# Kernel tuning notes

Hardware: AMD Instinct MI355X
Metric: run time of the kernel (lower is better)

The kernel has to match this reference:

```python
import jax, jax.numpy as jnp
import numpy as np

E, B, T = 7, 50, 100               # ensemble (network_size), no_batches=50, time blocks
D, A, L, H, C = 128, 32, 256, 1024, 128  # data, action, latent, hidden, context sizes
H_STEP = 0.1                        # (t1 - t0) / T == dt -> one SDE step per block


def setup_inputs() -> dict:
    key = jax.random.key(0)
    ks = iter(jax.random.split(key, 64))
    def nrm(shape, scale=1.0):
        return jax.random.normal(next(ks), shape, jnp.float32) * scale
    def ens(i, o):
        s = 1.0 / np.sqrt(i)
        return nrm((E, i, o), s), nrm((E, o), s)
    def lin(i, o):
        s = 1.0 / np.sqrt(i)
        return nrm((i, o), s), nrm((o,), s)
    inp = {}
    inp["enc_w1"], inp["enc_b1"] = ens(D, H)
    inp["enc_w2"], inp["enc_b2"] = ens(H, H)
    inp["enc_w3"], inp["enc_b3"] = ens(H, C)
    inp["qz0_w"], inp["qz0_b"] = ens(C, 2 * L)
    inp["act_w"], inp["act_b"] = ens(L + A + D, L)
    inp["proj_w1"], inp["proj_b1"] = ens(L, H)
    inp["proj_w2"], inp["proj_b2"] = ens(H, H)
    inp["proj_w3"], inp["proj_b3"] = ens(H, D)
    inp["f_w1"], inp["f_b1"] = lin(L, H)
    inp["f_w2"], inp["f_b2"] = lin(H, H)
    inp["f_w3"], inp["f_b3"] = lin(H, L)
    inp["h_w1"], inp["h_b1"] = lin(L, H)
    inp["h_w2"], inp["h_b2"] = lin(H, H)
    inp["h_w3"], inp["h_b3"] = lin(H, L)
    # per-latent-dim g nets: Linear(1,H) -> ReLU -> Linear(H,1), stacked over L dims
    inp["g_w1"] = nrm((L, H), 0.2)
    inp["g_b1"] = nrm((L, H), 0.2)
    inp["g_w2"] = nrm((L, H), 0.2 / np.sqrt(H))
    inp["g_b2"] = 0.5 + nrm((L,), 0.01)   # keep diffusion bounded away from 0
    inp["pz0_mean"] = jnp.zeros((E, 1, L), jnp.float32)
    inp["pz0_logstd"] = jnp.zeros((E, 1, L), jnp.float32)
    inp["xs"] = nrm((E, T * B, D))
    inp["actions"] = nrm((E, T * B, A))
    inp["eps_z0"] = nrm((T, E, B, L))      # torch.randn_like noise for z0 reparam
    inp["dw_noise"] = nrm((T, E * B, L))   # Brownian increment noise (unit std)
    return inp


def reference(enc_w1, enc_b1, enc_w2, enc_b2, enc_w3, enc_b3,
              qz0_w, qz0_b, act_w, act_b,
              proj_w1, proj_b1, proj_w2, proj_b2, proj_w3, proj_b3,
              f_w1, f_b1, f_w2, f_b2, f_w3, f_b3,
              h_w1, h_b1, h_w2, h_b2, h_w3, h_b3,
              g_w1, g_b1, g_w2, g_b2,
              pz0_mean, pz0_logstd,
              xs, actions, eps_z0, dw_noise):
    def ens_lin(x, w, b):  # EnsembleFC: bmm + bias
        return jnp.einsum('ebi,eio->ebo', x, w) + b[:, None, :]

    def encoder(x):
        x = jax.nn.relu(ens_lin(x, enc_w1, enc_b1))
        x = jax.nn.relu(ens_lin(x, enc_w2, enc_b2))
        return ens_lin(x, enc_w3, enc_b3)

    def projector(z):
        z = jnp.tanh(ens_lin(z, proj_w1, proj_b1))
        z = jnp.tanh(ens_lin(z, proj_w2, proj_b2))
        return ens_lin(z, proj_w3, proj_b3)

    def mlp(y, w1, b1, w2, b2, w3, b3):  # Linear-ReLU-Linear-Tanh-Linear
        y = jax.nn.relu(y @ w1 + b1)
        y = jnp.tanh(y @ w2 + b2)
        return y @ w3 + b3

    def g_fn(y):  # vectorized per-dim tiny MLPs: y (N, L) -> (N, L)
        hh = jax.nn.relu(y[:, :, None] * g_w1[None] + g_b1[None])  # (N, L, H)
        return jnp.sum(hh * g_w2[None], axis=-1) + g_b2

    xs_t = jnp.moveaxis(xs.reshape(E, T, B, D), 1, 0)        # (T, E, B, D)
    act_t = jnp.moveaxis(actions.reshape(E, T, B, A), 1, 0)  # (T, E, B, A)
    sqrt_h = jnp.sqrt(jnp.float32(H_STEP))

    def step(carry, inps):
        zs_last, i = carry
        x_i, a_i, eps_i, dw_i = inps
        ctx = encoder(x_i)                                  # (E, B, C)
        q = ens_lin(ctx, qz0_w, qz0_b)                      # (E, B, 2L)
        qm, ql = q[..., :L], q[..., L:]
        z0 = qm + jnp.exp(ql) * eps_i
        z_in = jnp.where(i == 0, z0, zs_last)               # first step uses z0
        lad = jnp.concatenate([z_in, a_i, x_i], axis=2)
        z = ens_lin(lad, act_w, act_b).reshape(E * B, L)
        # one SDE step with logqp (f: posterior drift, h: prior drift, g: diffusion)
        fv = mlp(z, f_w1, f_b1, f_w2, f_b2, f_w3, f_b3)
        hv = mlp(z, h_w1, h_b1, h_w2, h_b2, h_w3, h_b3)
        gv = g_fn(z)
        u = (fv - hv) / gv
        lr = 0.5 * jnp.sum(u * u, axis=-1) * H_STEP         # (E*B,) log-ratio increment
        z_new = z + fv * H_STEP + gv * (sqrt_h * dw_i)
        zs_new = z_new.reshape(E, B, L)
        xm = projector(zs_new)                              # (E, B, D)
        # KL(q(z0) || p(z0)) for diagonal Gaussians
        kl = (pz0_logstd - ql) \
             + (jnp.exp(2.0 * ql) + (qm - pz0_mean) ** 2) / (2.0 * jnp.exp(2.0 * pz0_logstd)) \
             - 0.5
        logqp0 = kl.sum(axis=2).mean(axis=1)                # (E,)
        lr_mean = lr.reshape(E, B).mean(axis=1)             # (E,)
        return (zs_new, i + 1), (lr_mean, logqp0, xm)

    init = (jnp.zeros((E, B, L), xs.dtype), jnp.int32(0))
    (_, _), (lrm, lq0, xms) = jax.lax.scan(step, init, (xs_t, act_t, eps_z0, dw_noise))
    logqp_path = lrm.sum(axis=0) + lq0.sum(axis=0)          # (E,)
    predicted_xs = jnp.moveaxis(xms, 0, 1).reshape(E, T * B, D)
    return logqp_path, predicted_xs
```

## Files before the change

### kernel.cpp

```cpp
#include <hip/hip_runtime.h>
#include <hip/hip_bf16.h>
#include <math.h>

#define E_ 7
#define B_ 50
#define T_ 100
#define D_ 128
#define A_ 32
#define L_ 256
#define H_ 1024
#define C_ 128
#define LAD_ 416
#define EB_ 350
#define TB_ 5000
#define SQRTH 0.31622776601683794f

typedef __attribute__((ext_vector_type(8))) short s8v;
typedef __attribute__((ext_vector_type(4))) float f32x4;
typedef __hip_bfloat16 bf16;

struct BG {
  const bf16* A[8];
  const bf16* W[8];
  const float* bias[8];
  float* Cf[8];
  bf16* Cb[8];
};

template<int BM, int ACT, int OUT>
__global__ __launch_bounds__(256)
void bgemm(BG g, int M, int K, int lda, int ldw, int ldc) {
  __shared__ short As[BM * 64];
  __shared__ short Ws[128 * 64];
  const short* Ap = (const short*)g.A[blockIdx.z];
  const short* Wp = (const short*)g.W[blockIdx.z];
  const int bm = blockIdx.x * BM, bn = blockIdx.y * 128;
  const int tid = threadIdx.x;
  const int wv = tid >> 6, lane = tid & 63;
  const int wm0 = (wv >> 1) * (BM / 2), wn0 = (wv & 1) * 64;
  const int l15 = lane & 15, l4 = lane >> 4;
  constexpr int FM = BM / 32;
  constexpr int AI = BM / 32;
  f32x4 acc[FM][4] = {};
  for (int k0 = 0; k0 < K; k0 += 64) {
    s8v av[AI], wvv[4];
#pragma unroll
    for (int i = 0; i < AI; ++i) {
      const int c = tid + i * 256, r = c >> 3, ck = c & 7;
      s8v v = {};
      if (bm + r < M) v = *(const s8v*)(Ap + (size_t)(bm + r) * lda + k0 + ck * 8);
      av[i] = v;
    }
#pragma unroll
    for (int i = 0; i < 4; ++i) {
      const int c = tid + i * 256, r = c >> 3, ck = c & 7;
      wvv[i] = *(const s8v*)(Wp + (size_t)(bn + r) * ldw + k0 + ck * 8);
    }
    __syncthreads();
#pragma unroll
    for (int i = 0; i < AI; ++i) {
      const int c = tid + i * 256, r = c >> 3, ck = c & 7;
      *(s8v*)(As + r * 64 + ((ck ^ (r & 7)) << 3)) = av[i];
    }
#pragma unroll
    for (int i = 0; i < 4; ++i) {
      const int c = tid + i * 256, r = c >> 3, ck = c & 7;
      *(s8v*)(Ws + r * 64 + ((ck ^ (r & 7)) << 3)) = wvv[i];
    }
    __syncthreads();
#pragma unroll
    for (int ks = 0; ks < 2; ++ks) {
      s8v af[FM], bfr[4];
#pragma unroll
      for (int m = 0; m < FM; ++m) {
        const int r = wm0 + m * 16 + l15, ck = ks * 4 + l4;
        af[m] = *(const s8v*)(As + r * 64 + ((ck ^ (r & 7)) << 3));
      }
#pragma unroll
      for (int n = 0; n < 4; ++n) {
        const int r = wn0 + n * 16 + l15, ck = ks * 4 + l4;
        bfr[n] = *(const s8v*)(Ws + r * 64 + ((ck ^ (r & 7)) << 3));
      }
#pragma unroll
      for (int m = 0; m < FM; ++m)
#pragma unroll
        for (int n = 0; n < 4; ++n)
          acc[m][n] = __builtin_amdgcn_mfma_f32_16x16x32_bf16(af[m], bfr[n], acc[m][n], 0, 0, 0);
    }
    __syncthreads();
  }
  const float* bias = g.bias[blockIdx.z];
  float* Cf = g.Cf[blockIdx.z];
  bf16* Cb = g.Cb[blockIdx.z];
#pragma unroll
  for (int n = 0; n < 4; ++n) {
    const int col = bn + wn0 + n * 16 + l15;
    const float bv = bias ? bias[col] : 0.f;
#pragma unroll
    for (int m = 0; m < FM; ++m) {
#pragma unroll
      for (int j = 0; j < 4; ++j) {
        const int row = bm + wm0 + m * 16 + l4 * 4 + j;
        if (row < M) {
          float v = acc[m][n][j] + bv;
          if (ACT == 1) v = fmaxf(v, 0.f);
          if (ACT == 2) v = tanhf(v);
          if (OUT == 0) Cf[(size_t)row * ldc + col] = v;
          if (OUT == 1) Cb[(size_t)row * ldc + col] = __float2bfloat16(v);
        }
      }
    }
  }
}

__global__ __launch_bounds__(256)
void cvtT_kernel(const float* __restrict__ src, bf16* __restrict__ dst,
                 int K, int N, long ss, long ds) {
  __shared__ float t[32][33];
  src += (size_t)blockIdx.z * ss;
  dst += (size_t)blockIdx.z * ds;
  const int n0 = blockIdx.x * 32, k0 = blockIdx.y * 32;
  const int tx = threadIdx.x & 31, ty = threadIdx.x >> 5;
#pragma unroll
  for (int i = 0; i < 4; ++i)
    t[ty + 8 * i][tx] = src[(size_t)(k0 + ty + 8 * i) * N + n0 + tx];
  __syncthreads();
#pragma unroll
  for (int i = 0; i < 4; ++i)
    dst[(size_t)(n0 + ty + 8 * i) * K + k0 + tx] = __float2bfloat16(t[tx][ty + 8 * i]);
}

struct B4 { bf16 a, b, c, d; };
__global__ __launch_bounds__(256)
void cvt_kernel(const float* __restrict__ s, bf16* __restrict__ d, int n4) {
  const int i = blockIdx.x * 256 + threadIdx.x;
  if (i < n4) {
    const float4 v = ((const float4*)s)[i];
    B4 o = {__float2bfloat16(v.x), __float2bfloat16(v.y),
            __float2bfloat16(v.z), __float2bfloat16(v.w)};
    ((B4*)d)[i] = o;
  }
}

__global__ __launch_bounds__(256)
void act_gemm(const float* __restrict__ zin, int zin_estride,
              const float* __restrict__ actions, const float* __restrict__ xs,
              const float* __restrict__ act_w, const float* __restrict__ act_b,
              float* __restrict__ zout, bf16* __restrict__ zout_bf, int t) {
  __shared__ float As[16][68];
  __shared__ float Bs[16][64];
  const int tid = threadIdx.x;
  const int e = blockIdx.y;
  const int bn = blockIdx.x * 64;
  const int tm = (tid >> 4) << 2;
  const int tn = (tid & 15) << 2;
  const int am = tid >> 2;
  const int ak = (tid & 3) << 2;
  const int bk = tid >> 4;
  const int bn4 = (tid & 15) << 2;
  const float* W = act_w + (size_t)e * LAD_ * L_;
  const float* zin_e = zin + (size_t)e * zin_estride;
  float acc[4][4] = {};
  for (int k0 = 0; k0 < LAD_; k0 += 16) {
    float4 av = make_float4(0.f, 0.f, 0.f, 0.f);
    const int k = k0 + ak;
    if (am < B_) {
      if (k < L_)
        av = *(const float4*)(zin_e + (size_t)am * L_ + k);
      else if (k < L_ + A_)
        av = *(const float4*)(actions + ((size_t)e * TB_ + (size_t)t * B_ + am) * A_ + (k - L_));
      else
        av = *(const float4*)(xs + ((size_t)e * TB_ + (size_t)t * B_ + am) * D_ + (k - L_ - A_));
    }
    const float4 wv = *(const float4*)(W + (size_t)(k0 + bk) * L_ + (bn + bn4));
    __syncthreads();
    As[ak + 0][am] = av.x; As[ak + 1][am] = av.y;
    As[ak + 2][am] = av.z; As[ak + 3][am] = av.w;
    *(float4*)&Bs[bk][bn4] = wv;
    __syncthreads();
#pragma unroll
    for (int kk = 0; kk < 16; ++kk) {
      const float4 a4 = *(const float4*)&As[kk][tm];
      const float4 b4 = *(const float4*)&Bs[kk][tn];
      const float ar[4] = {a4.x, a4.y, a4.z, a4.w};
      const float br[4] = {b4.x, b4.y, b4.z, b4.w};
#pragma unroll
      for (int i = 0; i < 4; ++i)
#pragma unroll
        for (int j = 0; j < 4; ++j)
          acc[i][j] = fmaf(ar[i], br[j], acc[i][j]);
    }
  }
#pragma unroll
  for (int i = 0; i < 4; ++i) {
    const int m = tm + i;
    if (m < B_) {
#pragma unroll
      for (int j = 0; j < 4; ++j) {
        const float v = acc[i][j] + act_b[(size_t)e * L_ + bn + tn + j];
        const size_t idx = ((size_t)e * B_ + m) * L_ + (bn + tn + j);
        zout[idx] = v;
        zout_bf[idx] = __float2bfloat16(v);
      }
    }
  }
}

__global__ __launch_bounds__(256)
void qkl_kernel(const float* __restrict__ ctx, int rows, int row_off, int ctx_estride,
                const float* __restrict__ qw, const float* __restrict__ qb,
                const float* __restrict__ pm, const float* __restrict__ pl,
                const float* __restrict__ eps0, float* __restrict__ z0,
                float* __restrict__ logqp) {
  __shared__ float cx[16][128];
  __shared__ float red[16];
  const int e = blockIdx.y;
  const int r0 = blockIdx.x * 16;
  const int tid = threadIdx.x;
  {
    const int r = tid >> 4, c = (tid & 15) * 8;
    float4 v0 = make_float4(0.f, 0.f, 0.f, 0.f), v1 = v0;
    if (r0 + r < rows) {
      const float* src = ctx + (size_t)e * ctx_estride + (size_t)(r0 + r) * C_ + c;
      v0 = *(const float4*)src;
      v1 = *(const float4*)(src + 4);
    }
    *(float4*)&cx[r][c] = v0;
    *(float4*)&cx[r][c + 4] = v1;
  }
  if (tid < 16) red[tid] = 0.f;
  __syncthreads();
  const int j = tid;
  const float* w = qw + (size_t)e * C_ * 512;
  float am_[16] = {};
  float al_[16] = {};
  for (int k0 = 0; k0 < C_; k0 += 4) {
    float wm[4], wl[4];
#pragma unroll
    for (int q = 0; q < 4; ++q) {
      wm[q] = w[(size_t)(k0 + q) * 512 + j];
      wl[q] = w[(size_t)(k0 + q) * 512 + 256 + j];
    }
#pragma unroll
    for (int r = 0; r < 16; ++r) {
      const float4 cv = *(const float4*)&cx[r][k0];
      const float cc[4] = {cv.x, cv.y, cv.z, cv.w};
#pragma unroll
      for (int q = 0; q < 4; ++q) {
        am_[r] = fmaf(cc[q], wm[q], am_[r]);
        al_[r] = fmaf(cc[q], wl[q], al_[r]);
      }
    }
  }
  const float qbm = qb[(size_t)e * 512 + j];
  const float qbl = qb[(size_t)e * 512 + 256 + j];
  const float pmv = pm[(size_t)e * L_ + j];
  const float plv = pl[(size_t)e * L_ + j];
  const float inv2e = 0.5f * expf(-2.f * plv);
#pragma unroll
  for (int r = 0; r < 16; ++r) {
    float kl = 0.f;
    if (r0 + r < rows) {
      const float qm_ = am_[r] + qbm;
      const float ql_ = al_[r] + qbl;
      const float dm = qm_ - pmv;
      kl = plv - ql_ + (expf(2.f * ql_) + dm * dm) * inv2e - 0.5f;
      const int gi = row_off + r0 + r;
      if (gi < B_) {
        const size_t zi = ((size_t)e * B_ + gi) * L_ + j;
        z0[zi] = qm_ + expf(ql_) * eps0[zi];
      }
    }
    for (int off = 32; off; off >>= 1) kl += __shfl_xor(kl, off, 64);
    if ((tid & 63) == 0) atomicAdd(&red[r], kl);
  }
  __syncthreads();
  if (tid < 16 && r0 + tid < rows) atomicAdd(&logqp[e], red[tid] * (1.0f / B_));
}

__global__ __launch_bounds__(64)
void g_kernel(const float* __restrict__ z, const float* __restrict__ gw1,
              const float* __restrict__ gb1, const float* __restrict__ gw2,
              const float* __restrict__ gb2, float* __restrict__ gv) {
  const int l = blockIdx.x;
  const int r0 = blockIdx.y * 44;
  const int rend = (r0 + 44 < EB_) ? (r0 + 44) : EB_;
  const int lane = threadIdx.x;
  float w1[16], b1[16], w2[16];
#pragma unroll
  for (int i = 0; i < 16; ++i) {
    const int h = lane + i * 64;
    w1[i] = gw1[(size_t)l * H_ + h];
    b1[i] = gb1[(size_t)l * H_ + h];
    w2[i] = gw2[(size_t)l * H_ + h];
  }
  const float g2 = gb2[l];
  for (int r = r0; r < rend; ++r) {
    const float zv = z[(size_t)r * L_ + l];
    float acc = 0.f;
#pragma unroll
    for (int i = 0; i < 16; ++i) {
      float hh = fmaf(zv, w1[i], b1[i]);
      hh = fmaxf(hh, 0.f);
      acc = fmaf(hh, w2[i], acc);
    }
    for (int off = 32; off; off >>= 1) acc += __shfl_xor(acc, off, 64);
    if (lane == 0) gv[(size_t)r * L_ + l] = acc + g2;
  }
}

__global__ __launch_bounds__(256)
void epi_kernel(const float* __restrict__ fvp, const float* __restrict__ fb3,
                const float* __restrict__ hb3, const float* __restrict__ gv,
                const float* __restrict__ z, const float* __restrict__ dw,
                float* __restrict__ zs_all, bf16* __restrict__ zs_bf,
                float* __restrict__ logqp, int t) {
  __shared__ float wsum[4];
  const int r = blockIdx.x;
  const int l = threadIdx.x;
  const int e = r / B_, b = r - e * B_;
  const size_t rl = (size_t)r * L_ + l;
  float fv = fb3[l], hv = hb3[l];
#pragma unroll
  for (int s = 0; s < 4; ++s) {
    fv += fvp[(size_t)s * EB_ * L_ + rl];
    hv += fvp[(size_t)(4 + s) * EB_ * L_ + rl];
  }
  const float gvv = gv[rl];
  const float u = (fv - hv) / gvv;
  float s_ = u * u;
  for (int off = 32; off; off >>= 1) s_ += __shfl_xor(s_, off, 64);
  if ((l & 63) == 0) wsum[l >> 6] = s_;
  __syncthreads();
  if (l == 0) {
    const float tot = wsum[0] + wsum[1] + wsum[2] + wsum[3];
    atomicAdd(&logqp[e], 0.5f * tot * 0.1f * (1.0f / B_));
  }
  const float znew = z[rl] + fv * 0.1f + gvv * (SQRTH * dw[(size_t)t * EB_ * L_ + rl]);
  const size_t oi = (((size_t)e * T_ + t) * B_ + b) * L_ + l;
  zs_all[oi] = znew;
  zs_bf[oi] = __float2bfloat16(znew);
}

__global__ void init_kernel(float* logqp) {
  if (threadIdx.x < E_) logqp[threadIdx.x] = 0.f;
}

extern "C" void kernel_launch(void* const* d_in, const int* in_sizes, int n_in,
                              void* d_out, int out_size, void* d_ws, size_t ws_size,
                              hipStream_t stream) {
  (void)in_sizes; (void)n_in; (void)out_size;
  const float* enc_w1 = (const float*)d_in[0];
  const float* enc_b1 = (const float*)d_in[1];
  const float* enc_w2 = (const float*)d_in[2];
  const float* enc_b2 = (const float*)d_in[3];
  const float* enc_w3 = (const float*)d_in[4];
  const float* enc_b3 = (const float*)d_in[5];
  const float* qz0_w  = (const float*)d_in[6];
  const float* qz0_b  = (const float*)d_in[7];
  const float* act_w  = (const float*)d_in[8];
  const float* act_b  = (const float*)d_in[9];
  const float* proj_w1 = (const float*)d_in[10];
  const float* proj_b1 = (const float*)d_in[11];
  const float* proj_w2 = (const float*)d_in[12];
  const float* proj_b2 = (const float*)d_in[13];
  const float* proj_w3 = (const float*)d_in[14];
  const float* proj_b3 = (const float*)d_in[15];
  const float* f_w1 = (const float*)d_in[16];
  const float* f_b1 = (const float*)d_in[17];
  const float* f_w2 = (const float*)d_in[18];
  const float* f_b2 = (const float*)d_in[19];
  const float* f_w3 = (const float*)d_in[20];
  const float* f_b3 = (const float*)d_in[21];
  const float* h_w1 = (const float*)d_in[22];
  const float* h_b1 = (const float*)d_in[23];
  const float* h_w2 = (const float*)d_in[24];
  const float* h_b2 = (const float*)d_in[25];
  const float* h_w3 = (const float*)d_in[26];
  const float* h_b3 = (const float*)d_in[27];
  const float* g_w1 = (const float*)d_in[28];
  const float* g_b1 = (const float*)d_in[29];
  const float* g_w2 = (const float*)d_in[30];
  const float* g_b2 = (const float*)d_in[31];
  const float* pz0_mean   = (const float*)d_in[32];
  const float* pz0_logstd = (const float*)d_in[33];
  const float* xs      = (const float*)d_in[34];
  const float* actions = (const float*)d_in[35];
  const float* eps_z0  = (const float*)d_in[36];
  const float* dw      = (const float*)d_in[37];

  float* out = (float*)d_out;
  float* logqp = out;
  float* pred = out + E_;

  char* base = (char*)d_ws;
  size_t off = 0;
  auto alloc = [&](size_t bytes) {
    void* p = base + off;
    off = (off + bytes + 255) & ~(size_t)255;
    return p;
  };
  float* zs_all = (float*)alloc((size_t)E_ * T_ * B_ * L_ * 4);
  bf16* zs_bf   = (bf16*)alloc((size_t)E_ * T_ * B_ * L_ * 2);
  float* z0     = (float*)alloc((size_t)E_ * B_ * L_ * 4);
  float* zbuf   = (float*)alloc((size_t)EB_ * L_ * 4);
  bf16* zbuf_bf = (bf16*)alloc((size_t)EB_ * L_ * 2);
  bf16* fh1     = (bf16*)alloc((size_t)2 * EB_ * H_ * 2);
  bf16* fh2     = (bf16*)alloc((size_t)2 * EB_ * H_ * 2);
  float* fvhvp  = (float*)alloc((size_t)8 * EB_ * L_ * 4);
  float* gvb    = (float*)alloc((size_t)EB_ * L_ * 4);
  bf16* xs_bf   = (bf16*)alloc((size_t)E_ * TB_ * D_ * 2);
  bf16* ew1T = (bf16*)alloc((size_t)E_ * D_ * H_ * 2);
  bf16* ew2T = (bf16*)alloc((size_t)E_ * H_ * H_ * 2);
  bf16* ew3T = (bf16*)alloc((size_t)E_ * H_ * C_ * 2);
  bf16* pw1T = (bf16*)alloc((size_t)E_ * L_ * H_ * 2);
  bf16* pw2T = (bf16*)alloc((size_t)E_ * H_ * H_ * 2);
  bf16* pw3T = (bf16*)alloc((size_t)E_ * H_ * D_ * 2);
  bf16* fw1T = (bf16*)alloc((size_t)L_ * H_ * 2);
  bf16* fw2T = (bf16*)alloc((size_t)H_ * H_ * 2);
  bf16* fw3T = (bf16*)alloc((size_t)H_ * L_ * 2);
  bf16* hw1T = (bf16*)alloc((size_t)L_ * H_ * 2);
  bf16* hw2T = (bf16*)alloc((size_t)H_ * H_ * 2);
  bf16* hw3T = (bf16*)alloc((size_t)H_ * L_ * 2);
  const size_t per_row = (size_t)E_ * (H_ * 2 * 2 + C_ * 4);
  size_t remain = (ws_size > off + 4096) ? (ws_size - off - 4096) : 0;
  int CH = (int)(remain / per_row);
  if (CH > 2500) CH = 2500;
  if (CH < 64) CH = 64;
  bf16* bufA = (bf16*)alloc((size_t)E_ * CH * H_ * 2);
  bf16* bufB = (bf16*)alloc((size_t)E_ * CH * H_ * 2);
  float* bufC = (float*)alloc((size_t)E_ * CH * C_ * 4);

  init_kernel<<<dim3(1), dim3(64), 0, stream>>>(logqp);

  const dim3 cb(256);
  cvt_kernel<<<dim3((E_ * TB_ * D_ / 4 + 255) / 256), cb, 0, stream>>>(xs, xs_bf, E_ * TB_ * D_ / 4);
  cvtT_kernel<<<dim3(H_ / 32, D_ / 32, E_), cb, 0, stream>>>(enc_w1, ew1T, D_, H_, (long)D_ * H_, (long)D_ * H_);
  cvtT_kernel<<<dim3(H_ / 32, H_ / 32, E_), cb, 0, stream>>>(enc_w2, ew2T, H_, H_, (long)H_ * H_, (long)H_ * H_);
  cvtT_kernel<<<dim3(C_ / 32, H_ / 32, E_), cb, 0, stream>>>(enc_w3, ew3T, H_, C_, (long)H_ * C_, (long)H_ * C_);
  cvtT_kernel<<<dim3(H_ / 32, L_ / 32, E_), cb, 0, stream>>>(proj_w1, pw1T, L_, H_, (long)L_ * H_, (long)L_ * H_);
  cvtT_kernel<<<dim3(H_ / 32, H_ / 32, E_), cb, 0, stream>>>(proj_w2, pw2T, H_, H_, (long)H_ * H_, (long)H_ * H_);
  cvtT_kernel<<<dim3(D_ / 32, H_ / 32, E_), cb, 0, stream>>>(proj_w3, pw3T, H_, D_, (long)H_ * D_, (long)H_ * D_);
  cvtT_kernel<<<dim3(H_ / 32, L_ / 32, 1), cb, 0, stream>>>(f_w1, fw1T, L_, H_, 0, 0);
  cvtT_kernel<<<dim3(H_ / 32, H_ / 32, 1), cb, 0, stream>>>(f_w2, fw2T, H_, H_, 0, 0);
  cvtT_kernel<<<dim3(L_ / 32, H_ / 32, 1), cb, 0, stream>>>(f_w3, fw3T, H_, L_, 0, 0);
  cvtT_kernel<<<dim3(H_ / 32, L_ / 32, 1), cb, 0, stream>>>(h_w1, hw1T, L_, H_, 0, 0);
  cvtT_kernel<<<dim3(H_ / 32, H_ / 32, 1), cb, 0, stream>>>(h_w2, hw2T, H_, H_, 0, 0);
  cvtT_kernel<<<dim3(L_ / 32, H_ / 32, 1), cb, 0, stream>>>(h_w3, hw3T, H_, L_, 0, 0);

  BG g;
  for (int c = 0; c < TB_; c += CH) {
    const int rows = (TB_ - c < CH) ? (TB_ - c) : CH;
    const int mt = (rows + 127) / 128;
    for (int e = 0; e < E_; ++e) {
      g.A[e] = xs_bf + ((size_t)e * TB_ + c) * D_;
      g.W[e] = ew1T + (size_t)e * D_ * H_;
      g.bias[e] = enc_b1 + (size_t)e * H_;
      g.Cb[e] = bufA + (size_t)e * CH * H_;
    }
    bgemm<128, 1, 1><<<dim3(mt, H_ / 128, E_), 256, 0, stream>>>(g, rows, D_, D_, D_, H_);
    for (int e = 0; e < E_; ++e) {
      g.A[e] = bufA + (size_t)e * CH * H_;
      g.W[e] = ew2T + (size_t)e * H_ * H_;
      g.bias[e] = enc_b2 + (size_t)e * H_;
      g.Cb[e] = bufB + (size_t)e * CH * H_;
    }
    bgemm<128, 1, 1><<<dim3(mt, H_ / 128, E_), 256, 0, stream>>>(g, rows, H_, H_, H_, H_);
    for (int e = 0; e < E_; ++e) {
      g.A[e] = bufB + (size_t)e * CH * H_;
      g.W[e] = ew3T + (size_t)e * H_ * C_;
      g.bias[e] = enc_b3 + (size_t)e * C_;
      g.Cf[e] = bufC + (size_t)e * CH * C_;
    }
    bgemm<128, 0, 0><<<dim3(mt, C_ / 128, E_), 256, 0, stream>>>(g, rows, H_, H_, H_, C_);
    qkl_kernel<<<dim3((rows + 15) / 16, E_), 256, 0, stream>>>(
        bufC, rows, c, CH * C_, qz0_w, qz0_b, pz0_mean, pz0_logstd, eps_z0, z0, logqp);
  }

  for (int t = 0; t < T_; ++t) {
    const float* zin;
    int zes;
    if (t == 0) { zin = z0; zes = B_ * L_; }
    else { zin = zs_all + (size_t)(t - 1) * B_ * L_; zes = T_ * B_ * L_; }
    act_gemm<<<dim3(L_ / 64, E_), 256, 0, stream>>>(zin, zes, actions, xs, act_w, act_b,
                                                    zbuf, zbuf_bf, t);
    g.A[0] = zbuf_bf; g.W[0] = fw1T; g.bias[0] = f_b1; g.Cb[0] = fh1;
    g.A[1] = zbuf_bf; g.W[1] = hw1T; g.bias[1] = h_b1; g.Cb[1] = fh1 + (size_t)EB_ * H_;
    bgemm<64, 1, 1><<<dim3(6, H_ / 128, 2), 256, 0, stream>>>(g, EB_, L_, L_, L_, H_);
    g.A[0] = fh1; g.W[0] = fw2T; g.bias[0] = f_b2; g.Cb[0] = fh2;
    g.A[1] = fh1 + (size_t)EB_ * H_; g.W[1] = hw2T; g.bias[1] = h_b2;
    g.Cb[1] = fh2 + (size_t)EB_ * H_;
    bgemm<64, 2, 1><<<dim3(6, H_ / 128, 2), 256, 0, stream>>>(g, EB_, H_, H_, H_, H_);
    for (int jj = 0; jj < 8; ++jj) {
      const int fb = jj >> 2, s = jj & 3;
      g.A[jj] = fh2 + (size_t)fb * EB_ * H_ + s * 256;
      g.W[jj] = (fb ? hw3T : fw3T) + s * 256;
      g.bias[jj] = nullptr;
      g.Cf[jj] = fvhvp + (size_t)jj * EB_ * L_;
    }
    bgemm<64, 0, 0><<<dim3(6, L_ / 128, 8), 256, 0, stream>>>(g, EB_, 256, H_, H_, L_);
    g_kernel<<<dim3(L_, 8), 64, 0, stream>>>(zbuf, g_w1, g_b1, g_w2, g_b2, gvb);
    epi_kernel<<<dim3(EB_), 256, 0, stream>>>(fvhvp, f_b3, h_b3, gvb, zbuf, dw,
                                              zs_all, zs_bf, logqp, t);
  }

  for (int c = 0; c < TB_; c += CH) {
    const int rows = (TB_ - c < CH) ? (TB_ - c) : CH;
    const int mt = (rows + 127) / 128;
    for (int e = 0; e < E_; ++e) {
      g.A[e] = zs_bf + ((size_t)e * T_ * B_ + c) * L_;
      g.W[e] = pw1T + (size_t)e * L_ * H_;
      g.bias[e] = proj_b1 + (size_t)e * H_;
      g.Cb[e] = bufA + (size_t)e * CH * H_;
    }
    bgemm<128, 2, 1><<<dim3(mt, H_ / 128, E_), 256, 0, stream>>>(g, rows, L_, L_, L_, H_);
    for (int e = 0; e < E_; ++e) {
      g.A[e] = bufA + (size_t)e * CH * H_;
      g.W[e] = pw2T + (size_t)e * H_ * H_;
      g.bias[e] = proj_b2 + (size_t)e * H_;
      g.Cb[e] = bufB + (size_t)e * CH * H_;
    }
    bgemm<128, 2, 1><<<dim3(mt, H_ / 128, E_), 256, 0, stream>>>(g, rows, H_, H_, H_, H_);
    for (int e = 0; e < E_; ++e) {
      g.A[e] = bufB + (size_t)e * CH * H_;
      g.W[e] = pw3T + (size_t)e * H_ * D_;
      g.bias[e] = proj_b3 + (size_t)e * D_;
      g.Cf[e] = pred + ((size_t)e * TB_ + c) * D_;
    }
    bgemm<128, 0, 0><<<dim3(mt, D_ / 128, E_), 256, 0, stream>>>(g, rows, H_, H_, H_, D_);
  }
}
```

Measured before the change: 11.16 ms.

## Restructure SDE time loop into four fused MFMA kernels with prepacked weights

Rewrites the per-timestep loop. The action/xs part of the action projection is precomputed for all timesteps with one batched GEMM. The z part uses split-bf16 (hi/lo) MFMA to keep near-fp32 accuracy. The f and h MLP layers are concatenated into single wide GEMMs over fragment-prepacked weights, and layer 3, the per-dim g network (fp16 packed), the log-ratio and the Euler update are fused into one kernel. This cuts per-step launches from six to four and removes the intermediate fvhvp/gv buffers, at the cost of more precomputation and lower-precision g evaluation.

```diff
diff --git a/kernel.cpp b/kernel.cpp
--- a/kernel.cpp
+++ b/kernel.cpp
@@ -10,14 +10,20 @@
 #define L_ 256
 #define H_ 1024
 #define C_ 128
-#define LAD_ 416
 #define EB_ 350
 #define TB_ 5000
 #define SQRTH 0.31622776601683794f
 
 typedef __attribute__((ext_vector_type(8))) short s8v;
 typedef __attribute__((ext_vector_type(4))) float f32x4;
+typedef _Float16 f16x2 __attribute__((ext_vector_type(2)));
 typedef __hip_bfloat16 bf16;
+
+#define MFMA __builtin_amdgcn_mfma_f32_16x16x32_bf16
+
+__device__ __forceinline__ int lswz(int row, int ck) {
+  return ((ck & ~7) | ((ck ^ row) & 7)) << 3;
+}
 
 struct BG {
   const bf16* A[8];
@@ -85,7 +91,7 @@
       for (int m = 0; m < FM; ++m)
 #pragma unroll
         for (int n = 0; n < 4; ++n)
-          acc[m][n] = __builtin_amdgcn_mfma_f32_16x16x32_bf16(af[m], bfr[n], acc[m][n], 0, 0, 0);
+          acc[m][n] = MFMA(af[m], bfr[n], acc[m][n], 0, 0, 0);
     }
     __syncthreads();
   }
@@ -143,75 +149,69 @@
 }
 
 __global__ __launch_bounds__(256)
-void act_gemm(const float* __restrict__ zin, int zin_estride,
-              const float* __restrict__ actions, const float* __restrict__ xs,
-              const float* __restrict__ act_w, const float* __restrict__ act_b,
-              float* __restrict__ zout, bf16* __restrict__ zout_bf, int t) {
-  __shared__ float As[16][68];
-  __shared__ float Bs[16][64];
-  const int tid = threadIdx.x;
-  const int e = blockIdx.y;
-  const int bn = blockIdx.x * 64;
-  const int tm = (tid >> 4) << 2;
-  const int tn = (tid & 15) << 2;
-  const int am = tid >> 2;
-  const int ak = (tid & 3) << 2;
-  const int bk = tid >> 4;
-  const int bn4 = (tid & 15) << 2;
-  const float* W = act_w + (size_t)e * LAD_ * L_;
-  const float* zin_e = zin + (size_t)e * zin_estride;
-  float acc[4][4] = {};
-  for (int k0 = 0; k0 < LAD_; k0 += 16) {
-    float4 av = make_float4(0.f, 0.f, 0.f, 0.f);
-    const int k = k0 + ak;
-    if (am < B_) {
-      if (k < L_)
-        av = *(const float4*)(zin_e + (size_t)am * L_ + k);
-      else if (k < L_ + A_)
-        av = *(const float4*)(actions + ((size_t)e * TB_ + (size_t)t * B_ + am) * A_ + (k - L_));
-      else
-        av = *(const float4*)(xs + ((size_t)e * TB_ + (size_t)t * B_ + am) * D_ + (k - L_ - A_));
-    }
-    const float4 wv = *(const float4*)(W + (size_t)(k0 + bk) * L_ + (bn + bn4));
-    __syncthreads();
-    As[ak + 0][am] = av.x; As[ak + 1][am] = av.y;
-    As[ak + 2][am] = av.z; As[ak + 3][am] = av.w;
-    *(float4*)&Bs[bk][bn4] = wv;
-    __syncthreads();
-#pragma unroll
-    for (int kk = 0; kk < 16; ++kk) {
-      const float4 a4 = *(const float4*)&As[kk][tm];
-      const float4 b4 = *(const float4*)&Bs[kk][tn];
-      const float ar[4] = {a4.x, a4.y, a4.z, a4.w};
-      const float br[4] = {b4.x, b4.y, b4.z, b4.w};
-#pragma unroll
-      for (int i = 0; i < 4; ++i)
-#pragma unroll
-        for (int j = 0; j < 4; ++j)
-          acc[i][j] = fmaf(ar[i], br[j], acc[i][j]);
-    }
-  }
-#pragma unroll
-  for (int i = 0; i < 4; ++i) {
-    const int m = tm + i;
-    if (m < B_) {
-#pragma unroll
-      for (int j = 0; j < 4; ++j) {
-        const float v = acc[i][j] + act_b[(size_t)e * L_ + bn + tn + j];
-        const size_t idx = ((size_t)e * B_ + m) * L_ + (bn + tn + j);
-        zout[idx] = v;
-        zout_bf[idx] = __float2bfloat16(v);
-      }
-    }
-  }
+void packW(const float* __restrict__ src, bf16* __restrict__ dst, int K, int N) {
+  const int idx = blockIdx.x * 256 + threadIdx.x;
+  if (idx >= K * N) return;
+  const int k = idx / N, n = idx - k * N;
+  const size_t fo = ((size_t)(n >> 4) * (K >> 5) + (k >> 5)) * 512 +
+                    (((k >> 3) & 3) << 7) + ((n & 15) << 3) + (k & 7);
+  dst[fo] = __float2bfloat16(src[idx]);
+}
+
+__global__ __launch_bounds__(256)
+void packWz(const float* __restrict__ act_w, bf16* __restrict__ hi, bf16* __restrict__ lo) {
+  const int idx = blockIdx.x * 256 + threadIdx.x;
+  if (idx >= E_ * 65536) return;
+  const int e = idx >> 16, rem = idx & 65535, k = rem >> 8, n = rem & 255;
+  const float w = act_w[(size_t)e * 416 * 256 + (size_t)k * 256 + n];
+  const bf16 h = __float2bfloat16(w);
+  const size_t fo = (size_t)e * 65536 + ((size_t)(n >> 4) * 8 + (k >> 5)) * 512 +
+                    (((k >> 3) & 3) << 7) + ((n & 15) << 3) + (k & 7);
+  hi[fo] = h;
+  lo[fo] = __float2bfloat16(w - __bfloat162float(h));
+}
+
+__global__ __launch_bounds__(256)
+void ax_build(const float* __restrict__ actions, const float* __restrict__ xs,
+              bf16* __restrict__ dst) {
+  const int idx = blockIdx.x * 256 + threadIdx.x;
+  if (idx >= E_ * TB_ * 192) return;
+  const int k = idx % 192;
+  const int r = (idx / 192) % TB_;
+  const int e = idx / (192 * TB_);
+  float v = 0.f;
+  if (k < 32) v = actions[((size_t)e * TB_ + r) * A_ + k];
+  else if (k < 160) v = xs[((size_t)e * TB_ + r) * D_ + (k - 32)];
+  dst[idx] = __float2bfloat16(v);
+}
+
+__global__ __launch_bounds__(256)
+void waxT_build(const float* __restrict__ act_w, bf16* __restrict__ dst) {
+  const int idx = blockIdx.x * 256 + threadIdx.x;
+  if (idx >= E_ * 256 * 192) return;
+  const int k = idx % 192;
+  const int n = (idx / 192) % 256;
+  const int e = idx / (192 * 256);
+  float v = (k < 160) ? act_w[(size_t)e * 416 * 256 + (size_t)(256 + k) * 256 + n] : 0.f;
+  dst[idx] = __float2bfloat16(v);
+}
+
+__global__ __launch_bounds__(256)
+void gpack_build(const float* __restrict__ gw1, const float* __restrict__ gb1,
+                 const float* __restrict__ gw2, _Float16* __restrict__ dst) {
+  const int idx = blockIdx.x * 256 + threadIdx.x;
+  if (idx >= 256 * 3 * 1024) return;
+  const int l = idx / 3072, rem = idx - l * 3072, arr = rem >> 10, h = rem & 1023;
+  const float* s = arr == 0 ? gw1 : (arr == 1 ? gb1 : gw2);
+  dst[idx] = (_Float16)s[(size_t)l * 1024 + h];
 }
 
 __global__ __launch_bounds__(256)
 void qkl_kernel(const float* __restrict__ ctx, int rows, int row_off, int ctx_estride,
                 const float* __restrict__ qw, const float* __restrict__ qb,
                 const float* __restrict__ pm, const float* __restrict__ pl,
-                const float* __restrict__ eps0, float* __restrict__ z0,
-                float* __restrict__ logqp) {
+                const float* __restrict__ eps0, bf16* __restrict__ z0hi,
+                bf16* __restrict__ z0lo, float* __restrict__ logqp) {
   __shared__ float cx[16][128];
   __shared__ float red[16];
   const int e = blockIdx.y;
@@ -268,7 +268,10 @@
       const int gi = row_off + r0 + r;
       if (gi < B_) {
         const size_t zi = ((size_t)e * B_ + gi) * L_ + j;
-        z0[zi] = qm_ + expf(ql_) * eps0[zi];
+        const float z0 = qm_ + expf(ql_) * eps0[zi];
+        const bf16 h = __float2bfloat16(z0);
+        z0hi[zi] = h;
+        z0lo[zi] = __float2bfloat16(z0 - __bfloat162float(h));
       }
     }
     for (int off = 32; off; off >>= 1) kl += __shfl_xor(kl, off, 64);
@@ -278,68 +281,266 @@
   if (tid < 16 && r0 + tid < rows) atomicAdd(&logqp[e], red[tid] * (1.0f / B_));
 }
 
-__global__ __launch_bounds__(64)
-void g_kernel(const float* __restrict__ z, const float* __restrict__ gw1,
-              const float* __restrict__ gb1, const float* __restrict__ gw2,
-              const float* __restrict__ gb2, float* __restrict__ gv) {
-  const int l = blockIdx.x;
-  const int r0 = blockIdx.y * 44;
-  const int rend = (r0 + 44 < EB_) ? (r0 + 44) : EB_;
-  const int lane = threadIdx.x;
-  float w1[16], b1[16], w2[16];
-#pragma unroll
-  for (int i = 0; i < 16; ++i) {
-    const int h = lane + i * 64;
-    w1[i] = gw1[(size_t)l * H_ + h];
-    b1[i] = gb1[(size_t)l * H_ + h];
-    w2[i] = gw2[(size_t)l * H_ + h];
-  }
-  const float g2 = gb2[l];
-  for (int r = r0; r < rend; ++r) {
-    const float zv = z[(size_t)r * L_ + l];
-    float acc = 0.f;
-#pragma unroll
-    for (int i = 0; i < 16; ++i) {
-      float hh = fmaf(zv, w1[i], b1[i]);
-      hh = fmaxf(hh, 0.f);
-      acc = fmaf(hh, w2[i], acc);
-    }
-    for (int off = 32; off; off >>= 1) acc += __shfl_xor(acc, off, 64);
-    if (lane == 0) gv[(size_t)r * L_ + l] = acc + g2;
-  }
-}
-
-__global__ __launch_bounds__(256)
-void epi_kernel(const float* __restrict__ fvp, const float* __restrict__ fb3,
-                const float* __restrict__ hb3, const float* __restrict__ gv,
-                const float* __restrict__ z, const float* __restrict__ dw,
-                float* __restrict__ zs_all, bf16* __restrict__ zs_bf,
-                float* __restrict__ logqp, int t) {
-  __shared__ float wsum[4];
-  const int r = blockIdx.x;
-  const int l = threadIdx.x;
-  const int e = r / B_, b = r - e * B_;
-  const size_t rl = (size_t)r * L_ + l;
-  float fv = fb3[l], hv = hb3[l];
-#pragma unroll
-  for (int s = 0; s < 4; ++s) {
-    fv += fvp[(size_t)s * EB_ * L_ + rl];
-    hv += fvp[(size_t)(4 + s) * EB_ * L_ + rl];
-  }
-  const float gvv = gv[rl];
-  const float u = (fv - hv) / gvv;
-  float s_ = u * u;
-  for (int off = 32; off; off >>= 1) s_ += __shfl_xor(s_, off, 64);
-  if ((l & 63) == 0) wsum[l >> 6] = s_;
-  __syncthreads();
-  if (l == 0) {
-    const float tot = wsum[0] + wsum[1] + wsum[2] + wsum[3];
-    atomicAdd(&logqp[e], 0.5f * tot * 0.1f * (1.0f / B_));
-  }
-  const float znew = z[rl] + fv * 0.1f + gvv * (SQRTH * dw[(size_t)t * EB_ * L_ + rl]);
-  const size_t oi = (((size_t)e * T_ + t) * B_ + b) * L_ + l;
-  zs_all[oi] = znew;
-  zs_bf[oi] = __float2bfloat16(znew);
+__global__ __launch_bounds__(256, 2)
+void k1_act(const bf16* __restrict__ zhi, const bf16* __restrict__ zlo,
+            const bf16* __restrict__ wzh, const bf16* __restrict__ wzl,
+            const float* __restrict__ axw, float* __restrict__ zP,
+            bf16* __restrict__ zPb, int t) {
+  __shared__ short Ah[16 * 256];
+  __shared__ short Al[16 * 256];
+  const int e = blockIdx.z, rb = blockIdx.x, nb = blockIdx.y * 128;
+  const int r0 = rb * 13;
+  const int nrows = (50 - r0 < 13) ? (50 - r0) : 13;
+  const int tid = threadIdx.x, lane = tid & 63, wv = tid >> 6;
+  const int l15 = lane & 15, l4 = lane >> 4;
+  const short* zh = (const short*)zhi + (size_t)(e * 50 + r0) * 256;
+  const short* zl = (const short*)zlo + (size_t)(e * 50 + r0) * 256;
+#pragma unroll
+  for (int i = 0; i < 2; ++i) {
+    const int lin = tid + i * 256, row = lin >> 5, ck = lin & 31;
+    s8v vh = {}, vl = {};
+    if (row < nrows) {
+      vh = *(const s8v*)(zh + row * 256 + ck * 8);
+      vl = *(const s8v*)(zl + row * 256 + ck * 8);
+    }
+    *(s8v*)(Ah + row * 256 + lswz(row, ck)) = vh;
+    *(s8v*)(Al + row * 256 + lswz(row, ck)) = vl;
+  }
+  __syncthreads();
+  const short* Bh = (const short*)wzh + (size_t)e * 65536;
+  const short* Bl = (const short*)wzl + (size_t)e * 65536;
+  f32x4 acc[2] = {};
+#pragma unroll
+  for (int kt = 0; kt < 8; ++kt) {
+    const int ck = kt * 4 + l4;
+    const s8v ah = *(const s8v*)(Ah + l15 * 256 + lswz(l15, ck));
+    const s8v al = *(const s8v*)(Al + l15 * 256 + lswz(l15, ck));
+#pragma unroll
+    for (int nt = 0; nt < 2; ++nt) {
+      const int ng = nb + wv * 32 + nt * 16;
+      const size_t bo = ((size_t)(ng >> 4) * 8 + kt) * 512 + lane * 8;
+      const s8v bh = *(const s8v*)(Bh + bo);
+      const s8v bl = *(const s8v*)(Bl + bo);
+      acc[nt] = MFMA(ah, bh, acc[nt], 0, 0, 0);
+      acc[nt] = MFMA(al, bh, acc[nt], 0, 0, 0);
+      acc[nt] = MFMA(ah, bl, acc[nt], 0, 0, 0);
+    }
+  }
+#pragma unroll
+  for (int nt = 0; nt < 2; ++nt) {
+    const int col = nb + wv * 32 + nt * 16 + l15;
+#pragma unroll
+    for (int j = 0; j < 4; ++j) {
+      const int row = l4 * 4 + j;
+      if (row < nrows) {
+        const int gr = e * 50 + r0 + row;
+        const float v = acc[nt][j] + axw[((size_t)e * TB_ + t * 50 + r0 + row) * 256 + col];
+        zP[(size_t)gr * 256 + col] = v;
+        zPb[(size_t)gr * 256 + col] = __float2bfloat16(v);
+      }
+    }
+  }
+}
+
+__global__ __launch_bounds__(256, 2)
+void k2_l1(const bf16* __restrict__ zPb, const bf16* __restrict__ w1f,
+           const float* __restrict__ fb1, const float* __restrict__ hb1,
+           bf16* __restrict__ fh1) {
+  __shared__ short As[16 * 256];
+  const int rb = blockIdx.x, nb = blockIdx.y * 128;
+  const int r0 = rb * 16;
+  const int tid = threadIdx.x, lane = tid & 63, wv = tid >> 6;
+  const int l15 = lane & 15, l4 = lane >> 4;
+#pragma unroll
+  for (int i = 0; i < 2; ++i) {
+    const int lin = tid + i * 256, row = lin >> 5, ck = lin & 31;
+    s8v v = {};
+    if (r0 + row < EB_)
+      v = *(const s8v*)((const short*)zPb + (size_t)(r0 + row) * 256 + ck * 8);
+    *(s8v*)(As + row * 256 + lswz(row, ck)) = v;
+  }
+  __syncthreads();
+  f32x4 acc[2] = {};
+#pragma unroll
+  for (int kt = 0; kt < 8; ++kt) {
+    const int ck = kt * 4 + l4;
+    const s8v a = *(const s8v*)(As + l15 * 256 + lswz(l15, ck));
+#pragma unroll
+    for (int nt = 0; nt < 2; ++nt) {
+      const int ng = nb + wv * 32 + nt * 16;
+      const s8v b = *(const s8v*)((const short*)w1f + ((size_t)(ng >> 4) * 8 + kt) * 512 + lane * 8);
+      acc[nt] = MFMA(a, b, acc[nt], 0, 0, 0);
+    }
+  }
+#pragma unroll
+  for (int nt = 0; nt < 2; ++nt) {
+    const int col = nb + wv * 32 + nt * 16 + l15;
+    const float bv = (col < 1024) ? fb1[col] : hb1[col - 1024];
+#pragma unroll
+    for (int j = 0; j < 4; ++j) {
+      const int row = r0 + l4 * 4 + j;
+      if (row < EB_)
+        fh1[(size_t)row * 2048 + col] = __float2bfloat16(fmaxf(acc[nt][j] + bv, 0.f));
+    }
+  }
+}
+
+__global__ __launch_bounds__(256, 2)
+void k3_l2(const bf16* __restrict__ fh1, const bf16* __restrict__ w2f,
+           const float* __restrict__ fb2, const float* __restrict__ hb2,
+           bf16* __restrict__ fh2) {
+  __shared__ short As[16 * 1024];
+  const int rb = blockIdx.x, nbl = blockIdx.y;
+  const int nb = nbl * 128, r0 = rb * 16;
+  const int half = (nbl >= 8) ? 1024 : 0;
+  const int tid = threadIdx.x, lane = tid & 63, wv = tid >> 6;
+  const int l15 = lane & 15, l4 = lane >> 4;
+#pragma unroll
+  for (int i = 0; i < 8; ++i) {
+    const int lin = tid + i * 256, row = lin >> 7, ck = lin & 127;
+    s8v v = {};
+    if (r0 + row < EB_)
+      v = *(const s8v*)((const short*)fh1 + (size_t)(r0 + row) * 2048 + half + ck * 8);
+    *(s8v*)(As + row * 1024 + lswz(row, ck)) = v;
+  }
+  __syncthreads();
+  f32x4 acc[2] = {};
+#pragma unroll 4
+  for (int kt = 0; kt < 32; ++kt) {
+    const int ck = kt * 4 + l4;
+    const s8v a = *(const s8v*)(As + l15 * 1024 + lswz(l15, ck));
+#pragma unroll
+    for (int nt = 0; nt < 2; ++nt) {
+      const int ng = nb + wv * 32 + nt * 16;
+      const s8v b = *(const s8v*)((const short*)w2f + ((size_t)(ng >> 4) * 32 + kt) * 512 + lane * 8);
+      acc[nt] = MFMA(a, b, acc[nt], 0, 0, 0);
+    }
+  }
+#pragma unroll
+  for (int nt = 0; nt < 2; ++nt) {
+    const int col = nb + wv * 32 + nt * 16 + l15;
+    const float bv = half ? hb2[col - 1024] : fb2[col];
+#pragma unroll
+    for (int j = 0; j < 4; ++j) {
+      const int row = r0 + l4 * 4 + j;
+      if (row < EB_)
+        fh2[(size_t)row * 2048 + col] = __float2bfloat16(tanhf(acc[nt][j] + bv));
+    }
+  }
+}
+
+__global__ __launch_bounds__(256, 1)
+void k4_fin(const bf16* __restrict__ fh2, const bf16* __restrict__ w3f,
+            const float* __restrict__ fb3, const float* __restrict__ hb3,
+            const _Float16* __restrict__ gpk, const float* __restrict__ gb2,
+            const float* __restrict__ zP, const float* __restrict__ dw,
+            bf16* __restrict__ zhi, bf16* __restrict__ zlo,
+            bf16* __restrict__ zs_bf, float* __restrict__ logqp, int t) {
+  __shared__ short As[16 * 1024];
+  __shared__ float ztile[16][64];
+  __shared__ float gvt[16][64];
+  __shared__ float ebuck[8];
+  const int rb = blockIdx.x, cb = blockIdx.y;
+  const int r0 = rb * 16, c0 = cb * 64;
+  const int tid = threadIdx.x, lane = tid & 63, wv = tid >> 6;
+  const int l15 = lane & 15, l4 = lane >> 4;
+  if (tid < 8) ebuck[tid] = 0.f;
+#pragma unroll
+  for (int i = 0; i < 4; ++i) {
+    const int lin = tid + i * 256, row = lin >> 6, col = lin & 63;
+    ztile[row][col] = (r0 + row < EB_) ? zP[(size_t)(r0 + row) * 256 + c0 + col] : 1.0f;
+  }
+  f32x4 accF = {}, accH = {};
+#pragma unroll
+  for (int fb = 0; fb < 2; ++fb) {
+    __syncthreads();
+#pragma unroll
+    for (int i = 0; i < 8; ++i) {
+      const int lin = tid + i * 256, row = lin >> 7, ck = lin & 127;
+      s8v v = {};
+      if (r0 + row < EB_)
+        v = *(const s8v*)((const short*)fh2 + (size_t)(r0 + row) * 2048 + fb * 1024 + ck * 8);
+      *(s8v*)(As + row * 1024 + lswz(row, ck)) = v;
+    }
+    __syncthreads();
+    const int ng = fb * 256 + c0 + wv * 16;
+    f32x4 acc = {};
+#pragma unroll 4
+    for (int kt = 0; kt < 32; ++kt) {
+      const int ck = kt * 4 + l4;
+      const s8v a = *(const s8v*)(As + l15 * 1024 + lswz(l15, ck));
+      const s8v b = *(const s8v*)((const short*)w3f + ((size_t)(ng >> 4) * 32 + kt) * 512 + lane * 8);
+      acc = MFMA(a, b, acc, 0, 0, 0);
+    }
+    if (fb) accH = acc; else accF = acc;
+  }
+  __syncthreads();
+  {
+    const int lloc = tid >> 2, hq = tid & 3;
+    const _Float16* gl = gpk + (size_t)(c0 + lloc) * 3072 + hq * 256;
+    f16x2 z2[16];
+#pragma unroll
+    for (int r = 0; r < 16; ++r) {
+      const _Float16 zh_ = (_Float16)ztile[r][lloc];
+      z2[r] = f16x2{zh_, zh_};
+    }
+    float ga[16] = {};
+    for (int hp = 0; hp < 128; ++hp) {
+      const f16x2 w1v = *(const f16x2*)(gl + 2 * hp);
+      const f16x2 b1v = *(const f16x2*)(gl + 1024 + 2 * hp);
+      const f16x2 w2v = *(const f16x2*)(gl + 2048 + 2 * hp);
+#pragma unroll
+      for (int r = 0; r < 16; ++r) {
+        f16x2 tt = z2[r] * w1v + b1v;
+#if __has_builtin(__builtin_elementwise_max)
+        const f16x2 zz = {};
+        tt = __builtin_elementwise_max(tt, zz);
+#else
+        tt[0] = tt[0] > (_Float16)0 ? tt[0] : (_Float16)0;
+        tt[1] = tt[1] > (_Float16)0 ? tt[1] : (_Float16)0;
+#endif
+#if __has_builtin(__builtin_amdgcn_fdot2)
+        ga[r] = __builtin_amdgcn_fdot2(tt, w2v, ga[r], false);
+#else
+        ga[r] += (float)tt[0] * (float)w2v[0] + (float)tt[1] * (float)w2v[1];
+#endif
+      }
+    }
+#pragma unroll
+    for (int r = 0; r < 16; ++r) {
+      float v = ga[r];
+      v += __shfl_xor(v, 1, 64);
+      v += __shfl_xor(v, 2, 64);
+      if (hq == 0) gvt[r][lloc] = v + gb2[c0 + lloc];
+    }
+  }
+  __syncthreads();
+  const int col_loc = wv * 16 + l15, col = c0 + col_loc;
+  const float fb3v = fb3[col], hb3v = hb3[col];
+#pragma unroll
+  for (int j = 0; j < 4; ++j) {
+    const int rl = l4 * 4 + j, row = r0 + rl;
+    if (row < EB_) {
+      const float fv = accF[j] + fb3v;
+      const float hv = accH[j] + hb3v;
+      const float gv = gvt[rl][col_loc];
+      const float u = (fv - hv) / gv;
+      atomicAdd(&ebuck[row / 50], 0.001f * u * u);
+      const float znew = ztile[rl][col_loc] + 0.1f * fv +
+                         gv * (SQRTH * dw[(size_t)t * (EB_ * 256) + (size_t)row * 256 + col]);
+      const bf16 h = __float2bfloat16(znew);
+      const size_t zi = (size_t)row * 256 + col;
+      zhi[zi] = h;
+      zlo[zi] = __float2bfloat16(znew - __bfloat162float(h));
+      const int e = row / 50, b = row - e * 50;
+      zs_bf[((size_t)e * TB_ + t * 50 + b) * 256 + col] = h;
+    }
+  }
+  __syncthreads();
+  if (tid < 7) {
+    const float v = ebuck[tid];
+    if (v != 0.f) atomicAdd(&logqp[tid], v);
+  }
 }
 
 __global__ void init_kernel(float* logqp) {
@@ -400,28 +601,29 @@
     off = (off + bytes + 255) & ~(size_t)255;
     return p;
   };
-  float* zs_all = (float*)alloc((size_t)E_ * T_ * B_ * L_ * 4);
-  bf16* zs_bf   = (bf16*)alloc((size_t)E_ * T_ * B_ * L_ * 2);
-  float* z0     = (float*)alloc((size_t)E_ * B_ * L_ * 4);
-  float* zbuf   = (float*)alloc((size_t)EB_ * L_ * 4);
-  bf16* zbuf_bf = (bf16*)alloc((size_t)EB_ * L_ * 2);
-  bf16* fh1     = (bf16*)alloc((size_t)2 * EB_ * H_ * 2);
-  bf16* fh2     = (bf16*)alloc((size_t)2 * EB_ * H_ * 2);
-  float* fvhvp  = (float*)alloc((size_t)8 * EB_ * L_ * 4);
-  float* gvb    = (float*)alloc((size_t)EB_ * L_ * 4);
-  bf16* xs_bf   = (bf16*)alloc((size_t)E_ * TB_ * D_ * 2);
+  bf16* zhi    = (bf16*)alloc((size_t)EB_ * 256 * 2);
+  bf16* zlo    = (bf16*)alloc((size_t)EB_ * 256 * 2);
+  float* zP    = (float*)alloc((size_t)EB_ * 256 * 4);
+  bf16* zPb    = (bf16*)alloc((size_t)EB_ * 256 * 2);
+  bf16* fh1    = (bf16*)alloc((size_t)EB_ * 2048 * 2);
+  bf16* fh2    = (bf16*)alloc((size_t)EB_ * 2048 * 2);
+  bf16* zs_bf  = (bf16*)alloc((size_t)E_ * T_ * B_ * 256 * 2);
+  float* axw   = (float*)alloc((size_t)E_ * TB_ * 256 * 4);
+  bf16* ax_bf  = (bf16*)alloc((size_t)E_ * TB_ * 192 * 2);
+  bf16* waxT   = (bf16*)alloc((size_t)E_ * 256 * 192 * 2);
+  bf16* wzh    = (bf16*)alloc((size_t)E_ * 65536 * 2);
+  bf16* wzl    = (bf16*)alloc((size_t)E_ * 65536 * 2);
+  bf16* w1f    = (bf16*)alloc((size_t)2048 * 256 * 2);
+  bf16* w2f    = (bf16*)alloc((size_t)2048 * 1024 * 2);
+  bf16* w3f    = (bf16*)alloc((size_t)512 * 1024 * 2);
+  _Float16* gpk = (_Float16*)alloc((size_t)256 * 3 * 1024 * 2);
+  bf16* xs_bf  = (bf16*)alloc((size_t)E_ * TB_ * D_ * 2);
   bf16* ew1T = (bf16*)alloc((size_t)E_ * D_ * H_ * 2);
   bf16* ew2T = (bf16*)alloc((size_t)E_ * H_ * H_ * 2);
   bf16* ew3T = (bf16*)alloc((size_t)E_ * H_ * C_ * 2);
   bf16* pw1T = (bf16*)alloc((size_t)E_ * L_ * H_ * 2);
   bf16* pw2T = (bf16*)alloc((size_t)E_ * H_ * H_ * 2);
   bf16* pw3T = (bf16*)alloc((size_t)E_ * H_ * D_ * 2);
-  bf16* fw1T = (bf16*)alloc((size_t)L_ * H_ * 2);
-  bf16* fw2T = (bf16*)alloc((size_t)H_ * H_ * 2);
-  bf16* fw3T = (bf16*)alloc((size_t)H_ * L_ * 2);
-  bf16* hw1T = (bf16*)alloc((size_t)L_ * H_ * 2);
-  bf16* hw2T = (bf16*)alloc((size_t)H_ * H_ * 2);
-  bf16* hw3T = (bf16*)alloc((size_t)H_ * L_ * 2);
   const size_t per_row = (size_t)E_ * (H_ * 2 * 2 + C_ * 4);
   size_t remain = (ws_size > off + 4096) ? (ws_size - off - 4096) : 0;
   int CH = (int)(remain / per_row);
@@ -433,22 +635,34 @@
 
   init_kernel<<<dim3(1), dim3(64), 0, stream>>>(logqp);
 
-  const dim3 cb(256);
-  cvt_kernel<<<dim3((E_ * TB_ * D_ / 4 + 255) / 256), cb, 0, stream>>>(xs, xs_bf, E_ * TB_ * D_ / 4);
-  cvtT_kernel<<<dim3(H_ / 32, D_ / 32, E_), cb, 0, stream>>>(enc_w1, ew1T, D_, H_, (long)D_ * H_, (long)D_ * H_);
-  cvtT_kernel<<<dim3(H_ / 32, H_ / 32, E_), cb, 0, stream>>>(enc_w2, ew2T, H_, H_, (long)H_ * H_, (long)H_ * H_);
-  cvtT_kernel<<<dim3(C_ / 32, H_ / 32, E_), cb, 0, stream>>>(enc_w3, ew3T, H_, C_, (long)H_ * C_, (long)H_ * C_);
-  cvtT_kernel<<<dim3(H_ / 32, L_ / 32, E_), cb, 0, stream>>>(proj_w1, pw1T, L_, H_, (long)L_ * H_, (long)L_ * H_);
-  cvtT_kernel<<<dim3(H_ / 32, H_ / 32, E_), cb, 0, stream>>>(proj_w2, pw2T, H_, H_, (long)H_ * H_, (long)H_ * H_);
-  cvtT_kernel<<<dim3(D_ / 32, H_ / 32, E_), cb, 0, stream>>>(proj_w3, pw3T, H_, D_, (long)H_ * D_, (long)H_ * D_);
-  cvtT_kernel<<<dim3(H_ / 32, L_ / 32, 1), cb, 0, stream>>>(f_w1, fw1T, L_, H_, 0, 0);
-  cvtT_kernel<<<dim3(H_ / 32, H_ / 32, 1), cb, 0, stream>>>(f_w2, fw2T, H_, H_, 0, 0);
-  cvtT_kernel<<<dim3(L_ / 32, H_ / 32, 1), cb, 0, stream>>>(f_w3, fw3T, H_, L_, 0, 0);
-  cvtT_kernel<<<dim3(H_ / 32, L_ / 32, 1), cb, 0, stream>>>(h_w1, hw1T, L_, H_, 0, 0);
-  cvtT_kernel<<<dim3(H_ / 32, H_ / 32, 1), cb, 0, stream>>>(h_w2, hw2T, H_, H_, 0, 0);
-  cvtT_kernel<<<dim3(L_ / 32, H_ / 32, 1), cb, 0, stream>>>(h_w3, hw3T, H_, L_, 0, 0);
+  const dim3 cb256(256);
+  cvt_kernel<<<dim3((E_ * TB_ * D_ / 4 + 255) / 256), cb256, 0, stream>>>(xs, xs_bf, E_ * TB_ * D_ / 4);
+  cvtT_kernel<<<dim3(H_ / 32, D_ / 32, E_), cb256, 0, stream>>>(enc_w1, ew1T, D_, H_, (long)D_ * H_, (long)D_ * H_);
+  cvtT_kernel<<<dim3(H_ / 32, H_ / 32, E_), cb256, 0, stream>>>(enc_w2, ew2T, H_, H_, (long)H_ * H_, (long)H_ * H_);
+  cvtT_kernel<<<dim3(C_ / 32, H_ / 32, E_), cb256, 0, stream>>>(enc_w3, ew3T, H_, C_, (long)H_ * C_, (long)H_ * C_);
+  cvtT_kernel<<<dim3(H_ / 32, L_ / 32, E_), cb256, 0, stream>>>(proj_w1, pw1T, L_, H_, (long)L_ * H_, (long)L_ * H_);
+  cvtT_kernel<<<dim3(H_ / 32, H_ / 32, E_), cb256, 0, stream>>>(proj_w2, pw2T, H_, H_, (long)H_ * H_, (long)H_ * H_);
+  cvtT_kernel<<<dim3(D_ / 32, H_ / 32, E_), cb256, 0, stream>>>(proj_w3, pw3T, H_, D_, (long)H_ * D_, (long)H_ * D_);
+  ax_build<<<dim3((E_ * TB_ * 192 + 255) / 256), cb256, 0, stream>>>(actions, xs, ax_bf);
+  waxT_build<<<dim3((E_ * 256 * 192 + 255) / 256), cb256, 0, stream>>>(act_w, waxT);
+  packWz<<<dim3((E_ * 65536 + 255) / 256), cb256, 0, stream>>>(act_w, wzh, wzl);
+  packW<<<dim3((256 * 1024 + 255) / 256), cb256, 0, stream>>>(f_w1, w1f, 256, 1024);
+  packW<<<dim3((256 * 1024 + 255) / 256), cb256, 0, stream>>>(h_w1, w1f + (size_t)1024 * 256, 256, 1024);
+  packW<<<dim3((1024 * 1024 + 255) / 256), cb256, 0, stream>>>(f_w2, w2f, 1024, 1024);
+  packW<<<dim3((1024 * 1024 + 255) / 256), cb256, 0, stream>>>(h_w2, w2f + (size_t)1024 * 1024, 1024, 1024);
+  packW<<<dim3((1024 * 256 + 255) / 256), cb256, 0, stream>>>(f_w3, w3f, 1024, 256);
+  packW<<<dim3((1024 * 256 + 255) / 256), cb256, 0, stream>>>(h_w3, w3f + (size_t)256 * 1024, 1024, 256);
+  gpack_build<<<dim3((256 * 3 * 1024 + 255) / 256), cb256, 0, stream>>>(g_w1, g_b1, g_w2, gpk);
 
   BG g;
+  for (int e = 0; e < E_; ++e) {
+    g.A[e] = ax_bf + (size_t)e * TB_ * 192;
+    g.W[e] = waxT + (size_t)e * 256 * 192;
+    g.bias[e] = act_b + (size_t)e * 256;
+    g.Cf[e] = axw + (size_t)e * TB_ * 256;
+  }
+  bgemm<128, 0, 0><<<dim3((TB_ + 127) / 128, 2, E_), 256, 0, stream>>>(g, TB_, 192, 192, 192, 256);
+
   for (int c = 0; c < TB_; c += CH) {
     const int rows = (TB_ - c < CH) ? (TB_ - c) : CH;
     const int mt = (rows + 127) / 128;
@@ -474,34 +688,16 @@
     }
     bgemm<128, 0, 0><<<dim3(mt, C_ / 128, E_), 256, 0, stream>>>(g, rows, H_, H_, H_, C_);
     qkl_kernel<<<dim3((rows + 15) / 16, E_), 256, 0, stream>>>(
-        bufC, rows, c, CH * C_, qz0_w, qz0_b, pz0_mean, pz0_logstd, eps_z0, z0, logqp);
+        bufC, rows, c, CH * C_, qz0_w, qz0_b, pz0_mean, pz0_logstd, eps_z0,
+        zhi, zlo, logqp);
   }
 
   for (int t = 0; t < T_; ++t) {
-    const float* zin;
-    int zes;
-    if (t == 0) { zin = z0; zes = B_ * L_; }
-    else { zin = zs_all + (size_t)(t - 1) * B_ * L_; zes = T_ * B_ * L_; }
-    act_gemm<<<dim3(L_ / 64, E_), 256, 0, stream>>>(zin, zes, actions, xs, act_w, act_b,
-                                                    zbuf, zbuf_bf, t);
-    g.A[0] = zbuf_bf; g.W[0] = fw1T; g.bias[0] = f_b1; g.Cb[0] = fh1;
-    g.A[1] = zbuf_bf; g.W[1] = hw1T; g.bias[1] = h_b1; g.Cb[1] = fh1 + (size_t)EB_ * H_;
-    bgemm<64, 1, 1><<<dim3(6, H_ / 128, 2), 256, 0, stream>>>(g, EB_, L_, L_, L_, H_);
-    g.A[0] = fh1; g.W[0] = fw2T; g.bias[0] = f_b2; g.Cb[0] = fh2;
-    g.A[1] = fh1 + (size_t)EB_ * H_; g.W[1] = hw2T; g.bias[1] = h_b2;
-    g.Cb[1] = fh2 + (size_t)EB_ * H_;
-    bgemm<64, 2, 1><<<dim3(6, H_ / 128, 2), 256, 0, stream>>>(g, EB_, H_, H_, H_, H_);
-    for (int jj = 0; jj < 8; ++jj) {
-      const int fb = jj >> 2, s = jj & 3;
-      g.A[jj] = fh2 + (size_t)fb * EB_ * H_ + s * 256;
-      g.W[jj] = (fb ? hw3T : fw3T) + s * 256;
-      g.bias[jj] = nullptr;
-      g.Cf[jj] = fvhvp + (size_t)jj * EB_ * L_;
-    }
-    bgemm<64, 0, 0><<<dim3(6, L_ / 128, 8), 256, 0, stream>>>(g, EB_, 256, H_, H_, L_);
-    g_kernel<<<dim3(L_, 8), 64, 0, stream>>>(zbuf, g_w1, g_b1, g_w2, g_b2, gvb);
-    epi_kernel<<<dim3(EB_), 256, 0, stream>>>(fvhvp, f_b3, h_b3, gvb, zbuf, dw,
-                                              zs_all, zs_bf, logqp, t);
+    k1_act<<<dim3(4, 2, E_), 256, 0, stream>>>(zhi, zlo, wzh, wzl, axw, zP, zPb, t);
+    k2_l1<<<dim3(22, 16), 256, 0, stream>>>(zPb, w1f, f_b1, h_b1, fh1);
+    k3_l2<<<dim3(22, 16), 256, 0, stream>>>(fh1, w2f, f_b2, h_b2, fh2);
+    k4_fin<<<dim3(22, 4), 256, 0, stream>>>(fh2, w3f, f_b3, h_b3, gpk, g_b2,
+                                            zP, dw, zhi, zlo, zs_bf, logqp, t);
   }
 
   for (int c = 0; c < TB_; c += CH) {
```

Measured after the change: 10.30 ms. 1.08x faster.
